# Kernel tuning notes

Hardware: AMD Instinct MI355X
Metric: run time of the kernel (lower is better)

## Reference

```python
import jax, jax.numpy as jnp
import numpy as np
from jax import lax


def setup_inputs() -> dict:
    key = jax.random.key(0)
    k1, k2 = jax.random.split(key)
    N, dim, m = 8192, 1024, 1024
    x = jax.random.normal(k1, (N, dim), dtype=jnp.float32)
    vectors = jax.random.normal(k2, (m, dim), dtype=jnp.float32) * 0.01
    bias = jnp.zeros((dim,), dtype=jnp.float32)
    return {"x": x, "vectors": vectors, "bias": bias}


def reference(x, vectors, bias):
    # Normalize each reflection vector to unit length: [m, d]
    v_normed = vectors / jnp.linalg.norm(vectors, axis=1, keepdims=True)

    def step(out, v):
        # out: [N, d], v: [d]
        proj = out @ v                       # [N]
        out = out - 2.0 * proj[:, None] * v  # rank-1 Householder update
        return out, None

    out, _ = lax.scan(step, x, v_normed)
    return out + bias
```

## Files before the change

kernel.cpp:

```cpp
#include <hip/hip_runtime.h>
#include <hip/hip_bf16.h>

typedef __attribute__((ext_vector_type(8))) short short8;
typedef __attribute__((ext_vector_type(4))) short s16x4;
typedef __attribute__((ext_vector_type(4))) float f32x4;

static __device__ inline short f2bf(float f) {
    unsigned u = __float_as_uint(f);
    unsigned r = (u + 0x7fffu + ((u >> 16) & 1u)) >> 16;
    return (short)r;
}
static __device__ inline float bf2f(short h) {
    return __uint_as_float(((unsigned)(unsigned short)h) << 16);
}

static __device__ inline int swz32(int row, int slot) {
    return row * 32 + ((slot ^ ((row >> 1) & 3)) << 3);
}
static __device__ inline int swz64(int row, int slot) {
    return row * 64 + ((slot ^ (row & 7)) << 3);
}

__global__ __launch_bounds__(256) void k_norms(const float* __restrict__ vec,
                                               float* __restrict__ inv, int dim) {
    int row = blockIdx.x * 4 + (threadIdx.x >> 6);
    int lane = threadIdx.x & 63;
    const float4* src = (const float4*)(vec + (size_t)row * dim);
    float ss = 0.f;
#pragma unroll
    for (int i = 0; i < 4; ++i) {
        float4 v = src[lane + 64 * i];
        ss += v.x * v.x + v.y * v.y + v.z * v.z + v.w * v.w;
    }
#pragma unroll
    for (int off = 32; off; off >>= 1) ss += __shfl_xor(ss, off, 64);
    if (lane == 0) inv[row] = 1.0f / sqrtf(ss);
}

__global__ __launch_bounds__(256) void k_prep2(const float* __restrict__ vec,
                                               const float* __restrict__ inv,
                                               short* __restrict__ Vh, short* __restrict__ Vl,
                                               short* __restrict__ Vth, short* __restrict__ Vtl,
                                               int m, int dim) {
    __shared__ float tile[32][33];
    int c0 = blockIdx.x * 32, r0 = blockIdx.y * 32;
    int t = threadIdx.x;
    int r = t >> 3, c4 = (t & 7) * 4;
    float iv = inv[r0 + r];
    float4 v = *(const float4*)&vec[(size_t)(r0 + r) * dim + c0 + c4];
    float f[4] = {v.x * iv, v.y * iv, v.z * iv, v.w * iv};
    s16x4 h, l;
#pragma unroll
    for (int q = 0; q < 4; ++q) {
        h[q] = f2bf(f[q]);
        l[q] = f2bf(f[q] - bf2f(h[q]));
        tile[r][c4 + q] = f[q];
    }
    *(s16x4*)&Vh[(size_t)(r0 + r) * dim + c0 + c4] = h;
    *(s16x4*)&Vl[(size_t)(r0 + r) * dim + c0 + c4] = l;
    __syncthreads();
    s16x4 th, tl;
#pragma unroll
    for (int q = 0; q < 4; ++q) {
        float ff = tile[c4 + q][r];
        th[q] = f2bf(ff);
        tl[q] = f2bf(ff - bf2f(th[q]));
    }
    *(s16x4*)&Vth[(size_t)(c0 + r) * m + r0 + c4] = th;
    *(s16x4*)&Vtl[(size_t)(c0 + r) * m + r0 + c4] = tl;
}

template<int MODE, int TRI>
__global__ __launch_bounds__(256) void k_nt64pc(
    const short* __restrict__ Ah, const short* __restrict__ Al,
    const short* __restrict__ Bh, const short* __restrict__ Bl,
    float* __restrict__ Cf, short* __restrict__ Ch, short* __restrict__ Cl,
    int K, int lda, int ldb, int ldc, int gw, int nTiles,
    const float* __restrict__ castX, short* __restrict__ castXh, int castN4) {
    __shared__ short As[2][2][64 * 32];
    __shared__ short Bs[2][2][64 * 32];
    int flat = blockIdx.x;
    if (flat >= nTiles) {
        int idx = (flat - nTiles) * 256 + threadIdx.x;
        int stride = (gridDim.x - nTiles) * 256;
        for (int i = idx; i < castN4; i += stride) {
            float4 v = ((const float4*)castX)[i];
            float f[4] = {v.x, v.y, v.z, v.w};
            s16x4 h;
#pragma unroll
            for (int q = 0; q < 4; ++q) h[q] = f2bf(f[q]);
            *(s16x4*)&castXh[(size_t)i * 4] = h;
        }
        return;
    }
    int i0 = (flat / gw) * 64, j0 = (flat % gw) * 64;
    if (TRI == 2 && j0 < i0) return;
    int KE = (TRI == 1) ? (j0 + 64) : K;
    int t = threadIdx.x, lane = t & 63, wave = t >> 6;
    int wr = wave >> 1, wc = wave & 1;
    int srow = t >> 2, slot = t & 3;
    int sofs = swz32(srow, slot);
    int gofs = slot * 8;
    const short* gA_h = &Ah[(size_t)(i0 + srow) * lda + gofs];
    const short* gA_l = &Al[(size_t)(i0 + srow) * lda + gofs];
    const short* gB_h = &Bh[(size_t)(j0 + srow) * ldb + gofs];
    const short* gB_l = &Bl[(size_t)(j0 + srow) * ldb + gofs];
    short8 pAh = *(const short8*)&gA_h[0];
    short8 pAl = *(const short8*)&gA_l[0];
    short8 pBh = *(const short8*)&gB_h[0];
    short8 pBl = *(const short8*)&gB_l[0];
    *(short8*)&As[0][0][sofs] = pAh;
    *(short8*)&As[0][1][sofs] = pAl;
    *(short8*)&Bs[0][0][sofs] = pBh;
    *(short8*)&Bs[0][1][sofs] = pBl;
    f32x4 acc[2][2] = {};
    int nIter = KE >> 5;
    int cur = 0;
    for (int it = 0; it < nIter; ++it) {
        __syncthreads();
        int kn = (it + 1) << 5;
        bool have = kn < KE;
        if (have) {
            pAh = *(const short8*)&gA_h[kn];
            pAl = *(const short8*)&gA_l[kn];
            pBh = *(const short8*)&gB_h[kn];
            pBl = *(const short8*)&gB_l[kn];
        }
        int g = lane >> 4;
        short8 ah[2], al2[2], bh[2], bl2[2];
#pragma unroll
        for (int i = 0; i < 2; ++i) {
            int ro = swz32(wr * 32 + i * 16 + (lane & 15), g);
            ah[i] = *(const short8*)&As[cur][0][ro];
            al2[i] = *(const short8*)&As[cur][1][ro];
        }
#pragma unroll
        for (int j = 0; j < 2; ++j) {
            int ro = swz32(wc * 32 + j * 16 + (lane & 15), g);
            bh[j] = *(const short8*)&Bs[cur][0][ro];
            bl2[j] = *(const short8*)&Bs[cur][1][ro];
        }
#pragma unroll
        for (int i = 0; i < 2; ++i)
#pragma unroll
            for (int j = 0; j < 2; ++j) {
                acc[i][j] = __builtin_amdgcn_mfma_f32_16x16x32_bf16(ah[i], bh[j], acc[i][j], 0, 0, 0);
                acc[i][j] = __builtin_amdgcn_mfma_f32_16x16x32_bf16(ah[i], bl2[j], acc[i][j], 0, 0, 0);
                acc[i][j] = __builtin_amdgcn_mfma_f32_16x16x32_bf16(al2[i], bh[j], acc[i][j], 0, 0, 0);
            }
        if (have) {
            *(short8*)&As[cur ^ 1][0][sofs] = pAh;
            *(short8*)&As[cur ^ 1][1][sofs] = pAl;
            *(short8*)&Bs[cur ^ 1][0][sofs] = pBh;
            *(short8*)&Bs[cur ^ 1][1][sofs] = pBl;
        }
        cur ^= 1;
    }
#pragma unroll
    for (int i = 0; i < 2; ++i)
#pragma unroll
        for (int j = 0; j < 2; ++j) {
            int row0 = i0 + wr * 32 + i * 16 + ((lane >> 4) << 2);
            int col = j0 + wc * 32 + j * 16 + (lane & 15);
#pragma unroll
            for (int r = 0; r < 4; ++r) {
                float v = acc[i][j][r];
                size_t idx = (size_t)(row0 + r) * ldc + col;
                if (MODE == 2) {
                    Ch[idx] = f2bf((((row0 + r) == col) ? 1.f : 0.f) - v);
                } else {
                    short h = f2bf(v);
                    short l = f2bf(v - bf2f(h));
                    Ch[idx] = h;
                    Cl[idx] = l;
                    if (MODE == 3) Cf[idx] = v;
                }
            }
        }
}

__global__ __launch_bounds__(256) void k_baseinv2(const float* __restrict__ G,
                                                  short* __restrict__ Th, short* __restrict__ Tl,
                                                  short* __restrict__ Tth, short* __restrict__ Ttl,
                                                  int m) {
    __shared__ float Rs[64 * 64];
    int d = blockIdx.x >> 4, g = blockIdx.x & 15;
    int b0 = d * 64;
    int t = threadIdx.x, lane = t & 63, wave = t >> 6;
    {
        int r = t >> 2, c00 = (t & 3) * 16;
#pragma unroll
        for (int q = 0; q < 4; ++q)
            *(float4*)&Rs[r * 64 + c00 + q * 4] =
                *(const float4*)&G[(size_t)(b0 + r) * m + b0 + c00 + q * 4];
    }
    __syncthreads();
    int c = g * 4 + wave;
    float x = 0.f;
    for (int r = c; r >= 0; --r) {
        float prod = Rs[r * 64 + lane] * x;
        float s = prod;
#pragma unroll
        for (int off = 32; off; off >>= 1) s += __shfl_xor(s, off, 64);
        if (lane == r) x = ((r == c) ? 2.f : 0.f) - 2.f * s;
    }
    short h = f2bf(x);
    short l = f2bf(x - bf2f(h));
    Th[(size_t)(b0 + lane) * m + b0 + c] = h;
    Tl[(size_t)(b0 + lane) * m + b0 + c] = l;
    Tth[(size_t)(b0 + c) * m + b0 + lane] = h;
    Ttl[(size_t)(b0 + c) * m + b0 + lane] = l;
}

__global__ __launch_bounds__(256) void k_tree64f(const float* __restrict__ G,
                                                 short* __restrict__ Th, short* __restrict__ Tl,
                                                 short* __restrict__ Tth, short* __restrict__ Ttl,
                                                 int m) {
    __shared__ float Gb[64 * 65];
    __shared__ float Ai[64 * 65];
    __shared__ float Ci[64 * 64];
    __shared__ float Tm[64 * 64];
    int p = blockIdx.x;
    int a0 = p * 128, c0 = a0 + 64;
    int t = threadIdx.x;
    {
        int r = t >> 2, c00 = (t & 3) * 16;
#pragma unroll
        for (int q = 0; q < 4; ++q) {
            *(float4*)&Gb[r * 65 + c00 + q * 4] =
                *(const float4*)&G[(size_t)(a0 + r) * m + c0 + c00 + q * 4];
            s16x4 ha = *(const s16x4*)&Th[(size_t)(a0 + r) * m + a0 + c00 + q * 4];
            s16x4 la = *(const s16x4*)&Tl[(size_t)(a0 + r) * m + a0 + c00 + q * 4];
            s16x4 hc = *(const s16x4*)&Th[(size_t)(c0 + r) * m + c0 + c00 + q * 4];
            s16x4 lc = *(const s16x4*)&Tl[(size_t)(c0 + r) * m + c0 + c00 + q * 4];
#pragma unroll
            for (int e = 0; e < 4; ++e) {
                Ai[r * 65 + c00 + q * 4 + e] = bf2f(ha[e]) + bf2f(la[e]);
                Ci[r * 64 + c00 + q * 4 + e] = bf2f(hc[e]) + bf2f(lc[e]);
            }
        }
    }
    __syncthreads();
    int tx = t & 15, ty = t >> 4;
    float acc[4][4] = {};
#pragma unroll 4
    for (int k = 0; k < 64; ++k) {
        float av[4], bv[4];
#pragma unroll
        for (int i = 0; i < 4; ++i) av[i] = Gb[(ty * 4 + i) * 65 + k];
#pragma unroll
        for (int j = 0; j < 4; ++j) bv[j] = Ci[k * 64 + tx * 4 + j];
#pragma unroll
        for (int i = 0; i < 4; ++i)
#pragma unroll
            for (int j = 0; j < 4; ++j) acc[i][j] += av[i] * bv[j];
    }
#pragma unroll
    for (int i = 0; i < 4; ++i)
#pragma unroll
        for (int j = 0; j < 4; ++j) Tm[(ty * 4 + i) * 64 + tx * 4 + j] = acc[i][j];
    __syncthreads();
    float acc2[4][4] = {};
#pragma unroll 4
    for (int k = 0; k < 64; ++k) {
        float av[4], bv[4];
#pragma unroll
        for (int i = 0; i < 4; ++i) av[i] = Ai[(ty * 4 + i) * 65 + k];
#pragma unroll
        for (int j = 0; j < 4; ++j) bv[j] = Tm[k * 64 + tx * 4 + j];
#pragma unroll
        for (int i = 0; i < 4; ++i)
#pragma unroll
            for (int j = 0; j < 4; ++j) acc2[i][j] += av[i] * bv[j];
    }
#pragma unroll
    for (int i = 0; i < 4; ++i)
#pragma unroll
        for (int j = 0; j < 4; ++j) {
            float v = -acc2[i][j];
            short h = f2bf(v);
            short l = f2bf(v - bf2f(h));
            int R = a0 + ty * 4 + i, C = c0 + tx * 4 + j;
            Th[(size_t)R * m + C] = h;
            Tl[(size_t)R * m + C] = l;
            Tth[(size_t)C * m + R] = h;
            Ttl[(size_t)C * m + R] = l;
        }
}

template<int PHASE>
__global__ __launch_bounds__(256) void k_trimm(
    const short* __restrict__ Ah, const short* __restrict__ Al,
    const short* __restrict__ Bh, const short* __restrict__ Bl,
    short* __restrict__ C1h, short* __restrict__ C1l,
    short* __restrict__ C2h, short* __restrict__ C2l,
    int m, int s) {
    __shared__ short As[2][64 * 32];
    __shared__ short Bs[2][64 * 32];
    int p = blockIdx.z;
    int a0 = 2 * p * s, c0 = a0 + s;
    int r0 = blockIdx.y * 64, ct = blockIdx.x * 64;
    int KS = (PHASE == 1) ? 0 : r0;
    int KE = (PHASE == 1) ? (ct + 64) : s;
    size_t tbase = (size_t)p * s * s;
    int t = threadIdx.x, lane = t & 63, wave = t >> 6;
    int wr = wave >> 1, wc = wave & 1;
    int srow = t >> 2, slot = t & 3;
    int sofs = swz32(srow, slot);
    int gofs = slot * 8;
    f32x4 acc[2][2] = {};
    for (int k0 = KS; k0 < KE; k0 += 32) {
        __syncthreads();
        if (PHASE == 1) {
            *(short8*)&As[0][sofs] = *(const short8*)&Ah[(size_t)(a0 + r0 + srow) * m + c0 + k0 + gofs];
            *(short8*)&As[1][sofs] = *(const short8*)&Al[(size_t)(a0 + r0 + srow) * m + c0 + k0 + gofs];
            *(short8*)&Bs[0][sofs] = *(const short8*)&Bh[(size_t)(c0 + ct + srow) * m + c0 + k0 + gofs];
            *(short8*)&Bs[1][sofs] = *(const short8*)&Bl[(size_t)(c0 + ct + srow) * m + c0 + k0 + gofs];
        } else {
            *(short8*)&As[0][sofs] = *(const short8*)&Ah[(size_t)(a0 + r0 + srow) * m + a0 + k0 + gofs];
            *(short8*)&As[1][sofs] = *(const short8*)&Al[(size_t)(a0 + r0 + srow) * m + a0 + k0 + gofs];
            *(short8*)&Bs[0][sofs] = *(const short8*)&Bh[tbase + (size_t)(ct + srow) * s + k0 + gofs];
            *(short8*)&Bs[1][sofs] = *(const short8*)&Bl[tbase + (size_t)(ct + srow) * s + k0 + gofs];
        }
        __syncthreads();
        int g = lane >> 4;
        short8 ah[2], al2[2], bh[2], bl2[2];
#pragma unroll
        for (int i = 0; i < 2; ++i) {
            int ro = swz32(wr * 32 + i * 16 + (lane & 15), g);
            ah[i] = *(const short8*)&As[0][ro];
            al2[i] = *(const short8*)&As[1][ro];
        }
#pragma unroll
        for (int j = 0; j < 2; ++j) {
            int ro = swz32(wc * 32 + j * 16 + (lane & 15), g);
            bh[j] = *(const short8*)&Bs[0][ro];
            bl2[j] = *(const short8*)&Bs[1][ro];
        }
#pragma unroll
        for (int i = 0; i < 2; ++i)
#pragma unroll
            for (int j = 0; j < 2; ++j) {
                acc[i][j] = __builtin_amdgcn_mfma_f32_16x16x32_bf16(ah[i], bh[j], acc[i][j], 0, 0, 0);
                acc[i][j] = __builtin_amdgcn_mfma_f32_16x16x32_bf16(ah[i], bl2[j], acc[i][j], 0, 0, 0);
                acc[i][j] = __builtin_amdgcn_mfma_f32_16x16x32_bf16(al2[i], bh[j], acc[i][j], 0, 0, 0);
            }
    }
#pragma unroll
    for (int i = 0; i < 2; ++i)
#pragma unroll
        for (int j = 0; j < 2; ++j) {
            int row0 = r0 + wr * 32 + i * 16 + ((lane >> 4) << 2);
            int col = ct + wc * 32 + j * 16 + (lane & 15);
#pragma unroll
            for (int r = 0; r < 4; ++r) {
                if (PHASE == 1) {
                    float v = acc[i][j][r];
                    short h = f2bf(v);
                    short l = f2bf(v - bf2f(h));
                    size_t idx = tbase + (size_t)col * s + row0 + r;
                    C1h[idx] = h;
                    C1l[idx] = l;
                } else {
                    float v = -acc[i][j][r];
                    short h = f2bf(v);
                    short l = f2bf(v - bf2f(h));
                    int R = a0 + row0 + r, Cc = c0 + col;
                    C1h[(size_t)R * m + Cc] = h;
                    C1l[(size_t)R * m + Cc] = l;
                    C2h[(size_t)Cc * m + R] = h;
                    C2l[(size_t)Cc * m + R] = l;
                }
            }
        }
}

__global__ __launch_bounds__(256) void k_apply3(const short* __restrict__ xh,
                                                const short* __restrict__ Qt,
                                                const float* __restrict__ bias,
                                                float* __restrict__ out, int dim) {
    __shared__ short As[128 * 64];
    __shared__ short Bs[128 * 64];
    int nwg = gridDim.x * gridDim.y;
    int flat = blockIdx.y * gridDim.x + blockIdx.x;
    int cpx = nwg >> 3;
    int L = (flat & 7) * cpx + (flat >> 3);
    int m0 = (L / gridDim.x) * 128, n0 = (L % gridDim.x) * 128;
    int t = threadIdx.x, lane = t & 63, wave = t >> 6;
    int wr = wave >> 1, wc = wave & 1;
    int sr = lane >> 3;
    int sslot = (lane & 7) ^ (sr & 7);
    f32x4 acc[4][4] = {};
    for (int k0 = 0; k0 < dim; k0 += 64) {
        __syncthreads();
#pragma unroll
        for (int q = 0; q < 4; ++q) {
            int rg = wave * 4 + q;
            int row = rg * 8 + sr;
            const short* gA = &xh[(size_t)(m0 + row) * dim + k0 + sslot * 8];
            const short* gB = &Qt[(size_t)(n0 + row) * dim + k0 + sslot * 8];
            __builtin_amdgcn_global_load_lds(
                (const __attribute__((address_space(1))) void*)gA,
                (__attribute__((address_space(3))) void*)&As[rg * 8 * 64], 16, 0, 0);
            __builtin_amdgcn_global_load_lds(
                (const __attribute__((address_space(1))) void*)gB,
                (__attribute__((address_space(3))) void*)&Bs[rg * 8 * 64], 16, 0, 0);
        }
        __syncthreads();
#pragma unroll
        for (int kk = 0; kk < 2; ++kk) {
            int g = kk * 4 + (lane >> 4);
            short8 af[4], bf_[4];
#pragma unroll
            for (int i = 0; i < 4; ++i)
                af[i] = *(const short8*)&As[swz64(wr * 64 + i * 16 + (lane & 15), g)];
#pragma unroll
            for (int j = 0; j < 4; ++j)
                bf_[j] = *(const short8*)&Bs[swz64(wc * 64 + j * 16 + (lane & 15), g)];
#pragma unroll
            for (int i = 0; i < 4; ++i)
#pragma unroll
                for (int j = 0; j < 4; ++j)
                    acc[i][j] = __builtin_amdgcn_mfma_f32_16x16x32_bf16(af[i], bf_[j], acc[i][j], 0, 0, 0);
        }
    }
#pragma unroll
    for (int i = 0; i < 4; ++i)
#pragma unroll
        for (int j = 0; j < 4; ++j) {
            int row = m0 + wr * 64 + i * 16 + (lane >> 4) * 4;
            int col = n0 + wc * 64 + j * 16 + (lane & 15);
            float b = bias[col];
#pragma unroll
            for (int r = 0; r < 4; ++r)
                out[(size_t)(row + r) * dim + col] = acc[i][j][r] + b;
        }
}

extern "C" void kernel_launch(void* const* d_in, const int* in_sizes, int n_in,
                              void* d_out, int out_size, void* d_ws, size_t ws_size,
                              hipStream_t stream) {
    const float* x = (const float*)d_in[0];
    const float* vec = (const float*)d_in[1];
    const float* bias = (const float*)d_in[2];
    float* out = (float*)d_out;

    int dim = in_sizes[2];
    int m = in_sizes[1] / dim;
    int n = in_sizes[0] / dim;

    const size_t MD = (size_t)m * dim;
    const size_t MM = (size_t)m * m;

    char* cur = (char*)d_ws;
    auto alloc_f = [&](size_t nelem) { float* p = (float*)cur; cur += nelem * 4; return p; };
    auto alloc_s = [&](size_t nelem) { short* p = (short*)cur; cur += nelem * 2; return p; };
    float* G    = alloc_f(MM);
    float* invn = alloc_f(m);
    short* Vh  = alloc_s(MD);
    short* Vl  = alloc_s(MD);
    short* Vth = alloc_s(MD);
    short* Vtl = alloc_s(MD);
    short* Gh  = alloc_s(MM);
    short* Gl  = alloc_s(MM);
    short* Th  = alloc_s(MM);
    short* Tl  = alloc_s(MM);
    short* Tth = alloc_s(MM);
    short* Ttl = alloc_s(MM);
    short* Wh  = alloc_s(MD);
    short* Wl  = alloc_s(MD);
    short* Qt  = alloc_s((size_t)dim * dim);
    short* tmph = alloc_s(MM / 2);
    short* tmpl = alloc_s(MM / 2);
    short* xh  = alloc_s((size_t)n * dim);

    int gw = m / 64;
    int nTiles = gw * gw;
    int castN4 = (int)((size_t)n * dim / 4);

    k_norms<<<m / 4, 256, 0, stream>>>(vec, invn, dim);
    k_prep2<<<dim3(dim / 32, m / 32), 256, 0, stream>>>(vec, invn, Vh, Vl, Vth, Vtl, m, dim);

    k_nt64pc<3, 2><<<nTiles + 512, 256, 0, stream>>>(Vh, Vl, Vh, Vl, G, Gh, Gl,
                                                     dim, dim, dim, m, gw, nTiles,
                                                     x, xh, castN4);
    k_baseinv2<<<(m / 64) * 16, 256, 0, stream>>>(G, Th, Tl, Tth, Ttl, m);
    k_tree64f<<<m / 128, 256, 0, stream>>>(G, Th, Tl, Tth, Ttl, m);
    for (int s = 128; s < m; s <<= 1) {
        dim3 g(s / 64, s / 64, m / (2 * s));
        k_trimm<1><<<g, 256, 0, stream>>>(Gh, Gl, Tth, Ttl, tmph, tmpl, nullptr, nullptr, m, s);
        k_trimm<2><<<g, 256, 0, stream>>>(Th, Tl, tmph, tmpl, Th, Tl, Tth, Ttl, m, s);
    }

    k_nt64pc<1, 1><<<(m / 64) * (dim / 64), 256, 0, stream>>>(Vth, Vtl, Tth, Ttl, nullptr, Wh, Wl,
                                                              m, m, m, m, m / 64, (m / 64) * (dim / 64),
                                                              nullptr, nullptr, 0);
    k_nt64pc<2, 0><<<(dim / 64) * (dim / 64), 256, 0, stream>>>(Vth, Vtl, Wh, Wl, nullptr, Qt, nullptr,
                                                                m, m, m, dim, dim / 64, (dim / 64) * (dim / 64),
                                                                nullptr, nullptr, 0);

    k_apply3<<<dim3(dim / 128, n / 128), 256, 0, stream>>>(xh, Qt, bias, out, dim);
}
```

Baseline: 164.4 us.

## Drop low-order bf16 split terms in setup GEMMs and fuse normalization prep

Removes the hi/lo bf16 split for V and W, so the Gram, W and Q GEMMs issue one or two MFMAs per tile step instead of three, and load and write less data. The norm and prep kernels merge into one kernel that normalizes, casts and transposes eight rows per block. This lowers the accuracy of the compact-WY setup (G, W and Q lose their error-compensation terms), which could matter for tolerance.

```diff
diff --git a/kernel.cpp b/kernel.cpp
--- a/kernel.cpp
+++ b/kernel.cpp
@@ -21,56 +21,56 @@
     return row * 64 + ((slot ^ (row & 7)) << 3);
 }
 
-__global__ __launch_bounds__(256) void k_norms(const float* __restrict__ vec,
-                                               float* __restrict__ inv, int dim) {
-    int row = blockIdx.x * 4 + (threadIdx.x >> 6);
-    int lane = threadIdx.x & 63;
-    const float4* src = (const float4*)(vec + (size_t)row * dim);
+__global__ __launch_bounds__(256) void k_prepall(const float* __restrict__ vec,
+                                                 short* __restrict__ Vh,
+                                                 short* __restrict__ Vth,
+                                                 int m, int dim) {
+    __shared__ float tile[8][1028];
+    __shared__ float ps[8][32];
+    __shared__ float invs[8];
+    int r0 = blockIdx.x * 8;
+    int t = threadIdx.x;
+    int rt = t >> 5, ct = t & 31;
     float ss = 0.f;
 #pragma unroll
-    for (int i = 0; i < 4; ++i) {
-        float4 v = src[lane + 64 * i];
+    for (int p = 0; p < 8; ++p) {
+        int c = p * 128 + ct * 4;
+        float4 v = *(const float4*)&vec[(size_t)(r0 + rt) * dim + c];
+        *(float4*)&tile[rt][c] = v;
         ss += v.x * v.x + v.y * v.y + v.z * v.z + v.w * v.w;
     }
-#pragma unroll
-    for (int off = 32; off; off >>= 1) ss += __shfl_xor(ss, off, 64);
-    if (lane == 0) inv[row] = 1.0f / sqrtf(ss);
-}
-
-__global__ __launch_bounds__(256) void k_prep2(const float* __restrict__ vec,
-                                               const float* __restrict__ inv,
-                                               short* __restrict__ Vh, short* __restrict__ Vl,
-                                               short* __restrict__ Vth, short* __restrict__ Vtl,
-                                               int m, int dim) {
-    __shared__ float tile[32][33];
-    int c0 = blockIdx.x * 32, r0 = blockIdx.y * 32;
-    int t = threadIdx.x;
-    int r = t >> 3, c4 = (t & 7) * 4;
-    float iv = inv[r0 + r];
-    float4 v = *(const float4*)&vec[(size_t)(r0 + r) * dim + c0 + c4];
-    float f[4] = {v.x * iv, v.y * iv, v.z * iv, v.w * iv};
-    s16x4 h, l;
-#pragma unroll
-    for (int q = 0; q < 4; ++q) {
-        h[q] = f2bf(f[q]);
-        l[q] = f2bf(f[q] - bf2f(h[q]));
-        tile[r][c4 + q] = f[q];
-    }
-    *(s16x4*)&Vh[(size_t)(r0 + r) * dim + c0 + c4] = h;
-    *(s16x4*)&Vl[(size_t)(r0 + r) * dim + c0 + c4] = l;
+    ps[rt][ct] = ss;
     __syncthreads();
-    s16x4 th, tl;
-#pragma unroll
-    for (int q = 0; q < 4; ++q) {
-        float ff = tile[c4 + q][r];
-        th[q] = f2bf(ff);
-        tl[q] = f2bf(ff - bf2f(th[q]));
-    }
-    *(s16x4*)&Vth[(size_t)(c0 + r) * m + r0 + c4] = th;
-    *(s16x4*)&Vtl[(size_t)(c0 + r) * m + r0 + c4] = tl;
-}
-
-template<int MODE, int TRI>
+    if (t < 8) {
+        float s = 0.f;
+#pragma unroll
+        for (int q = 0; q < 32; ++q) s += ps[t][q];
+        invs[t] = 1.0f / sqrtf(s);
+    }
+    __syncthreads();
+    float iv = invs[rt];
+#pragma unroll
+    for (int p = 0; p < 8; ++p) {
+        int c = p * 128 + ct * 4;
+        s16x4 h;
+#pragma unroll
+        for (int q = 0; q < 4; ++q) h[q] = f2bf(tile[rt][c + q] * iv);
+        *(s16x4*)&Vh[(size_t)(r0 + rt) * dim + c] = h;
+    }
+#pragma unroll
+    for (int cc = 0; cc < 4; ++cc) {
+        int c = t * 4 + cc;
+        s16x4 h0, h1;
+#pragma unroll
+        for (int r = 0; r < 4; ++r) h0[r] = f2bf(tile[r][c] * invs[r]);
+#pragma unroll
+        for (int r = 0; r < 4; ++r) h1[r] = f2bf(tile[4 + r][c] * invs[4 + r]);
+        *(s16x4*)&Vth[(size_t)c * m + r0] = h0;
+        *(s16x4*)&Vth[(size_t)c * m + r0 + 4] = h1;
+    }
+}
+
+template<int MODE, int TRI, int CH>
 __global__ __launch_bounds__(256) void k_nt64pc(
     const short* __restrict__ Ah, const short* __restrict__ Al,
     const short* __restrict__ Bh, const short* __restrict__ Bl,
@@ -102,17 +102,18 @@
     int sofs = swz32(srow, slot);
     int gofs = slot * 8;
     const short* gA_h = &Ah[(size_t)(i0 + srow) * lda + gofs];
-    const short* gA_l = &Al[(size_t)(i0 + srow) * lda + gofs];
+    const short* gA_l = (CH >= 3) ? &Al[(size_t)(i0 + srow) * lda + gofs] : nullptr;
     const short* gB_h = &Bh[(size_t)(j0 + srow) * ldb + gofs];
-    const short* gB_l = &Bl[(size_t)(j0 + srow) * ldb + gofs];
+    const short* gB_l = (CH >= 2) ? &Bl[(size_t)(j0 + srow) * ldb + gofs] : nullptr;
     short8 pAh = *(const short8*)&gA_h[0];
-    short8 pAl = *(const short8*)&gA_l[0];
+    short8 pAl, pBl;
     short8 pBh = *(const short8*)&gB_h[0];
-    short8 pBl = *(const short8*)&gB_l[0];
+    if (CH >= 2) pBl = *(const short8*)&gB_l[0];
+    if (CH >= 3) pAl = *(const short8*)&gA_l[0];
     *(short8*)&As[0][0][sofs] = pAh;
-    *(short8*)&As[0][1][sofs] = pAl;
     *(short8*)&Bs[0][0][sofs] = pBh;
-    *(short8*)&Bs[0][1][sofs] = pBl;
+    if (CH >= 2) *(short8*)&Bs[0][1][sofs] = pBl;
+    if (CH >= 3) *(short8*)&As[0][1][sofs] = pAl;
     f32x4 acc[2][2] = {};
     int nIter = KE >> 5;
     int cur = 0;
@@ -122,9 +123,9 @@
         bool have = kn < KE;
         if (have) {
             pAh = *(const short8*)&gA_h[kn];
-            pAl = *(const short8*)&gA_l[kn];
             pBh = *(const short8*)&gB_h[kn];
-            pBl = *(const short8*)&gB_l[kn];
+            if (CH >= 2) pBl = *(const short8*)&gB_l[kn];
+            if (CH >= 3) pAl = *(const short8*)&gA_l[kn];
         }
         int g = lane >> 4;
         short8 ah[2], al2[2], bh[2], bl2[2];
@@ -132,27 +133,29 @@
         for (int i = 0; i < 2; ++i) {
             int ro = swz32(wr * 32 + i * 16 + (lane & 15), g);
             ah[i] = *(const short8*)&As[cur][0][ro];
-            al2[i] = *(const short8*)&As[cur][1][ro];
+            if (CH >= 3) al2[i] = *(const short8*)&As[cur][1][ro];
         }
 #pragma unroll
         for (int j = 0; j < 2; ++j) {
             int ro = swz32(wc * 32 + j * 16 + (lane & 15), g);
             bh[j] = *(const short8*)&Bs[cur][0][ro];
-            bl2[j] = *(const short8*)&Bs[cur][1][ro];
+            if (CH >= 2) bl2[j] = *(const short8*)&Bs[cur][1][ro];
         }
 #pragma unroll
         for (int i = 0; i < 2; ++i)
 #pragma unroll
             for (int j = 0; j < 2; ++j) {
                 acc[i][j] = __builtin_amdgcn_mfma_f32_16x16x32_bf16(ah[i], bh[j], acc[i][j], 0, 0, 0);
-                acc[i][j] = __builtin_amdgcn_mfma_f32_16x16x32_bf16(ah[i], bl2[j], acc[i][j], 0, 0, 0);
-                acc[i][j] = __builtin_amdgcn_mfma_f32_16x16x32_bf16(al2[i], bh[j], acc[i][j], 0, 0, 0);
+                if (CH >= 2)
+                    acc[i][j] = __builtin_amdgcn_mfma_f32_16x16x32_bf16(ah[i], bl2[j], acc[i][j], 0, 0, 0);
+                if (CH >= 3)
+                    acc[i][j] = __builtin_amdgcn_mfma_f32_16x16x32_bf16(al2[i], bh[j], acc[i][j], 0, 0, 0);
             }
         if (have) {
             *(short8*)&As[cur ^ 1][0][sofs] = pAh;
-            *(short8*)&As[cur ^ 1][1][sofs] = pAl;
             *(short8*)&Bs[cur ^ 1][0][sofs] = pBh;
-            *(short8*)&Bs[cur ^ 1][1][sofs] = pBl;
+            if (CH >= 2) *(short8*)&Bs[cur ^ 1][1][sofs] = pBl;
+            if (CH >= 3) *(short8*)&As[cur ^ 1][1][sofs] = pAl;
         }
         cur ^= 1;
     }
@@ -168,12 +171,13 @@
                 size_t idx = (size_t)(row0 + r) * ldc + col;
                 if (MODE == 2) {
                     Ch[idx] = f2bf((((row0 + r) == col) ? 1.f : 0.f) - v);
+                } else if (MODE == 1) {
+                    Ch[idx] = f2bf(v);
                 } else {
                     short h = f2bf(v);
-                    short l = f2bf(v - bf2f(h));
                     Ch[idx] = h;
-                    Cl[idx] = l;
-                    if (MODE == 3) Cf[idx] = v;
+                    Cl[idx] = f2bf(v - bf2f(h));
+                    Cf[idx] = v;
                 }
             }
         }
@@ -455,12 +459,9 @@
     char* cur = (char*)d_ws;
     auto alloc_f = [&](size_t nelem) { float* p = (float*)cur; cur += nelem * 4; return p; };
     auto alloc_s = [&](size_t nelem) { short* p = (short*)cur; cur += nelem * 2; return p; };
-    float* G    = alloc_f(MM);
-    float* invn = alloc_f(m);
+    float* G   = alloc_f(MM);
     short* Vh  = alloc_s(MD);
-    short* Vl  = alloc_s(MD);
     short* Vth = alloc_s(MD);
-    short* Vtl = alloc_s(MD);
     short* Gh  = alloc_s(MM);
     short* Gl  = alloc_s(MM);
     short* Th  = alloc_s(MM);
@@ -468,7 +469,6 @@
     short* Tth = alloc_s(MM);
     short* Ttl = alloc_s(MM);
     short* Wh  = alloc_s(MD);
-    short* Wl  = alloc_s(MD);
     short* Qt  = alloc_s((size_t)dim * dim);
     short* tmph = alloc_s(MM / 2);
     short* tmpl = alloc_s(MM / 2);
@@ -478,12 +478,11 @@
     int nTiles = gw * gw;
     int castN4 = (int)((size_t)n * dim / 4);
 
-    k_norms<<<m / 4, 256, 0, stream>>>(vec, invn, dim);
-    k_prep2<<<dim3(dim / 32, m / 32), 256, 0, stream>>>(vec, invn, Vh, Vl, Vth, Vtl, m, dim);
-
-    k_nt64pc<3, 2><<<nTiles + 512, 256, 0, stream>>>(Vh, Vl, Vh, Vl, G, Gh, Gl,
-                                                     dim, dim, dim, m, gw, nTiles,
-                                                     x, xh, castN4);
+    k_prepall<<<m / 8, 256, 0, stream>>>(vec, Vh, Vth, m, dim);
+
+    k_nt64pc<3, 2, 1><<<nTiles + 512, 256, 0, stream>>>(Vh, nullptr, Vh, nullptr, G, Gh, Gl,
+                                                        dim, dim, dim, m, gw, nTiles,
+                                                        x, xh, castN4);
     k_baseinv2<<<(m / 64) * 16, 256, 0, stream>>>(G, Th, Tl, Tth, Ttl, m);
     k_tree64f<<<m / 128, 256, 0, stream>>>(G, Th, Tl, Tth, Ttl, m);
     for (int s = 128; s < m; s <<= 1) {
@@ -492,12 +491,12 @@
         k_trimm<2><<<g, 256, 0, stream>>>(Th, Tl, tmph, tmpl, Th, Tl, Tth, Ttl, m, s);
     }
 
-    k_nt64pc<1, 1><<<(m / 64) * (dim / 64), 256, 0, stream>>>(Vth, Vtl, Tth, Ttl, nullptr, Wh, Wl,
-                                                              m, m, m, m, m / 64, (m / 64) * (dim / 64),
-                                                              nullptr, nullptr, 0);
-    k_nt64pc<2, 0><<<(dim / 64) * (dim / 64), 256, 0, stream>>>(Vth, Vtl, Wh, Wl, nullptr, Qt, nullptr,
-                                                                m, m, m, dim, dim / 64, (dim / 64) * (dim / 64),
-                                                                nullptr, nullptr, 0);
+    k_nt64pc<1, 1, 2><<<(m / 64) * (dim / 64), 256, 0, stream>>>(Vth, nullptr, Tth, Ttl, nullptr, Wh, nullptr,
+                                                                 m, m, m, m, m / 64, (m / 64) * (dim / 64),
+                                                                 nullptr, nullptr, 0);
+    k_nt64pc<2, 0, 1><<<(dim / 64) * (dim / 64), 256, 0, stream>>>(Vth, nullptr, Wh, nullptr, nullptr, Qt, nullptr,
+                                                                   m, m, m, dim, dim / 64, (dim / 64) * (dim / 64),
+                                                                   nullptr, nullptr, 0);
 
     k_apply3<<<dim3(dim / 128, n / 128), 256, 0, stream>>>(xh, Qt, bias, out, dim);
 }
```

After: 150.1 us. 8.7% less time.
